# Performance work log

Hardware: AMD Instinct MI355X
Metric: run time of the kernel (lower is better)

The kernel has to match this reference:

```python
import jax, jax.numpy as jnp
import numpy as np

VOXEL = 0.1  # voxel size used in NSLoss.voxelize


def _chamfer(x, y):
    """Squared-distance chamfer terms. x: [B,N,3], y: [B,M,3].
    Returns (dist1 [B,N]: min over y for each x point, dist2 [B,M])."""
    xx = jnp.sum(x * x, axis=-1)              # [B,N]
    yy = jnp.sum(y * y, axis=-1)              # [B,M]
    zz = jnp.einsum('bnd,bmd->bnm', x, y)     # [B,N,M]
    P = xx[:, :, None] + yy[None if False else slice(None), None, :][0] if False else xx[:, :, None] + yy[:, None, :] - 2.0 * zz
    return P.min(axis=2), P.min(axis=1)


def _voxelize(coord):
    # masked_fill(nan -> inf), per-batch min over points, quantize, truncate to int
    c = jnp.where(jnp.isnan(coord), jnp.inf, coord)
    gmin = c.min(axis=1, keepdims=True)       # [B,1,3]
    grid = ((coord - gmin) / VOXEL).astype(jnp.int32)  # trunc like torch .int()
    return jax.lax.stop_gradient(grid)        # torch .int() detaches grad


def setup_inputs() -> dict:
    key = jax.random.key(0)
    k1, k2 = jax.random.split(key)
    preds = jax.random.normal(k1, (2, 8192, 3), dtype=jnp.float32)
    gts = jax.random.normal(k2, (2, 8192, 3), dtype=jnp.float32)
    return {"preds": preds, "gts": gts}


def reference(preds, gts):
    # chamfer on raw coordinates
    d1, d2 = _chamfer(preds, gts)
    loss2 = d1.mean() + d2.mean()
    # chamfer on voxelized coordinates
    pv = _voxelize(preds).astype(jnp.float32)
    gv = _voxelize(gts).astype(jnp.float32)
    d1v, d2v = _chamfer(pv, gv)
    loss1 = d1v.mean() + d2v.mean()
    return loss1 + loss2
```

## Files before the change

kernel.cpp:

```cpp
#include <hip/hip_runtime.h>
#include <math.h>

#define B 2
#define N 8192
#define PTS_STRIDE (N*3)
#define VOXEL 0.1f

#define BLK  512
#define PBLK 1024
#define XPB 64
#define XTILES (N/XPB)
#define NBLOCKS (XTILES*4)

#define WS_GMIN 0
#define WS_ACC 16
#define WS_TICKET 17
#define OFF_PACK 32
#define PERG 147456
#define OFF_AFLO(g) (OFF_PACK + (g)*PERG)
#define OFF_AFHI(g) (OFF_AFLO(g) + 32768)
#define OFF_BR(g)   (OFF_AFLO(g) + 65536)
#define OFF_BV(g)   (OFF_AFLO(g) + 98304)
#define OFF_XXR(g)  (OFF_AFLO(g) + 131072)
#define OFF_XXV(g)  (OFF_AFLO(g) + 139264)

typedef __attribute__((ext_vector_type(8))) short short8;
typedef __attribute__((ext_vector_type(16))) float f16v;

union S8 { short8 v; unsigned short u[8]; };

__device__ __forceinline__ unsigned short f2bf(float f) {
    unsigned u = __float_as_uint(f);
    return (unsigned short)((u + 0x7FFFu + ((u >> 16) & 1u)) >> 16);
}
__device__ __forceinline__ float bf2f(unsigned short h) {
    return __uint_as_float(((unsigned)h) << 16);
}
__device__ __forceinline__ float voxq(float v, float g) {
    return (float)(int)((v - g) / VOXEL);
}

__global__ void __launch_bounds__(PBLK)
gmin_kernel(const float* __restrict__ preds,
            const float* __restrict__ gts,
            float* __restrict__ ws) {
    const int g   = blockIdx.x;
    const int arr = g >> 1;
    const int b   = g & 1;
    const float* base = (arr ? gts : preds) + b * PTS_STRIDE;

    float m0 = INFINITY, m1 = INFINITY, m2 = INFINITY;
    for (int i = threadIdx.x; i < N; i += PBLK) {
        float v0 = base[i*3+0], v1 = base[i*3+1], v2 = base[i*3+2];
        v0 = (v0 != v0) ? INFINITY : v0;
        v1 = (v1 != v1) ? INFINITY : v1;
        v2 = (v2 != v2) ? INFINITY : v2;
        m0 = fminf(m0, v0); m1 = fminf(m1, v1); m2 = fminf(m2, v2);
    }
    for (int off = 32; off; off >>= 1) {
        m0 = fminf(m0, __shfl_down(m0, off));
        m1 = fminf(m1, __shfl_down(m1, off));
        m2 = fminf(m2, __shfl_down(m2, off));
    }
    __shared__ float sm[16][3];
    const int wave = threadIdx.x >> 6, lane = threadIdx.x & 63;
    if (lane == 0) { sm[wave][0] = m0; sm[wave][1] = m1; sm[wave][2] = m2; }
    __syncthreads();
    if (threadIdx.x == 0) {
        float a0 = sm[0][0], a1 = sm[0][1], a2 = sm[0][2];
        for (int w = 1; w < 16; ++w) {
            a0 = fminf(a0, sm[w][0]);
            a1 = fminf(a1, sm[w][1]);
            a2 = fminf(a2, sm[w][2]);
        }
        ws[WS_GMIN + g*3+0] = a0; ws[WS_GMIN + g*3+1] = a1; ws[WS_GMIN + g*3+2] = a2;
        if (g == 0) { ws[WS_ACC] = 0.0f; ((unsigned*)ws)[WS_TICKET] = 0u; }
    }
}

__global__ void __launch_bounds__(256)
pack_kernel(const float* __restrict__ preds,
            const float* __restrict__ gts,
            float* __restrict__ ws) {
    const int i   = blockIdx.x * 256 + threadIdx.x;
    const int g   = i >> 13;
    const int idx = i & (N-1);
    const int arr = g >> 1;
    const int b   = g & 1;
    const float* base = (arr ? gts : preds) + b * PTS_STRIDE;

    const float g0 = ws[WS_GMIN + g*3+0];
    const float g1 = ws[WS_GMIN + g*3+1];
    const float g2 = ws[WS_GMIN + g*3+2];

    const float p0 = base[idx*3+0], p1 = base[idx*3+1], p2 = base[idx*3+2];
    const float w0 = voxq(p0, g0), w1 = voxq(p1, g1), w2 = voxq(p2, g2);
    const float rr = fmaf(p0,p0, fmaf(p1,p1, p2*p2));
    const float vv = fmaf(w0,w0, fmaf(w1,w1, w2*w2));

    const unsigned short yyh = f2bf(rr);
    const unsigned short yyl = f2bf(rr - bf2f(yyh));
    const unsigned short vvh = f2bf(vv);
    const unsigned short vvl = f2bf(vv - bf2f(vvh));
    const unsigned short ONE = 0x3F80;

    short8* AFLO = (short8*)(ws + OFF_AFLO(g));
    short8* AFHI = (short8*)(ws + OFF_AFHI(g));
    short8* BR   = (short8*)(ws + OFF_BR(g));
    short8* BV   = (short8*)(ws + OFF_BV(g));

    S8 f;
    f.u[0]=f2bf(p0); f.u[1]=f2bf(p1); f.u[2]=f2bf(p2);
    f.u[3]=yyh; f.u[4]=yyl; f.u[5]=f2bf(w0); f.u[6]=f2bf(w1); f.u[7]=f2bf(w2);
    AFLO[idx] = f.v;
    f.u[0]=vvh; f.u[1]=vvl; f.u[2]=0; f.u[3]=0; f.u[4]=0; f.u[5]=0; f.u[6]=0; f.u[7]=0;
    AFHI[idx] = f.v;
    f.u[0]=f2bf(-2.0f*p0); f.u[1]=f2bf(-2.0f*p1); f.u[2]=f2bf(-2.0f*p2);
    f.u[3]=ONE; f.u[4]=ONE; f.u[5]=0; f.u[6]=0; f.u[7]=0;
    BR[idx] = f.v;
    f.u[0]=0; f.u[1]=0; f.u[2]=0; f.u[3]=0; f.u[4]=0;
    f.u[5]=f2bf(-2.0f*w0); f.u[6]=f2bf(-2.0f*w1); f.u[7]=f2bf(-2.0f*w2);
    BV[idx] = f.v;
    ws[OFF_XXR(g) + idx] = rr;
    ws[OFF_XXV(g) + idx] = vv;
}

__global__ void __launch_bounds__(BLK, 4)
chamfer_kernel(float* __restrict__ ws, float* __restrict__ out) {
    const int tid  = threadIdx.x;
    const int wave = tid >> 6, lane = tid & 63;
    const int half = lane >> 5, c32 = lane & 31;
    const int slot = blockIdx.y;
    const int dir  = slot & 1;
    const int b    = slot >> 1;
    const int gX = dir*2 + b;
    const int gY = (1-dir)*2 + b;

    const short8* ALO = (const short8*)(ws + OFF_AFLO(gY));
    const short8* AHI = (const short8*)(ws + OFF_AFHI(gY));
    const short8* Abase = half ? AHI : ALO;
    const short8* BR = (const short8*)(ws + OFF_BR(gX));
    const short8* BV = (const short8*)(ws + OFF_BV(gX));

    __shared__ float smin[8][4][32];
    __shared__ float ssum[2];

    const int xbase = blockIdx.x * XPB;
    short8 bf[4];
    S8 hc;
    hc.u[0] = (c32 < 16) ? (unsigned short)0 : (unsigned short)0x3F80;
    hc.u[1] = hc.u[0];
    hc.u[2]=0; hc.u[3]=0; hc.u[4]=0; hc.u[5]=0; hc.u[6]=0; hc.u[7]=0;
#pragma unroll
    for (int f = 0; f < 4; ++f) {
        const int xi = xbase + f*16 + (c32 & 15);
        bf[f] = (half == 0) ? ((c32 < 16) ? BR[xi] : BV[xi]) : hc.v;
    }

    float mn0 = INFINITY, mn1 = INFINITY, mn2 = INFINITY, mn3 = INFINITY;
    const f16v Z = (f16v)(0.0f);
    const int abase0 = wave * 1024 + c32;

#pragma unroll 2
    for (int t = 0; t < 32; ++t) {
        const short8 a = Abase[abase0 + t*32];
        const f16v d0 = __builtin_amdgcn_mfma_f32_32x32x16_bf16(a, bf[0], Z, 0, 0, 0);
        const f16v d1 = __builtin_amdgcn_mfma_f32_32x32x16_bf16(a, bf[1], Z, 0, 0, 0);
        const f16v d2 = __builtin_amdgcn_mfma_f32_32x32x16_bf16(a, bf[2], Z, 0, 0, 0);
        const f16v d3 = __builtin_amdgcn_mfma_f32_32x32x16_bf16(a, bf[3], Z, 0, 0, 0);
#pragma unroll
        for (int r = 0; r < 16; r += 4) {
            mn0 = fminf(mn0, fminf(fminf(d0[r], d0[r+1]), fminf(d0[r+2], d0[r+3])));
            mn1 = fminf(mn1, fminf(fminf(d1[r], d1[r+1]), fminf(d1[r+2], d1[r+3])));
            mn2 = fminf(mn2, fminf(fminf(d2[r], d2[r+1]), fminf(d2[r+2], d2[r+3])));
            mn3 = fminf(mn3, fminf(fminf(d3[r], d3[r+1]), fminf(d3[r+2], d3[r+3])));
        }
    }

    mn0 = fminf(mn0, __shfl_xor(mn0, 32));
    mn1 = fminf(mn1, __shfl_xor(mn1, 32));
    mn2 = fminf(mn2, __shfl_xor(mn2, 32));
    mn3 = fminf(mn3, __shfl_xor(mn3, 32));
    if (half == 0) {
        smin[wave][0][c32] = mn0;
        smin[wave][1][c32] = mn1;
        smin[wave][2][c32] = mn2;
        smin[wave][3][c32] = mn3;
    }
    __syncthreads();

    if (tid < 128) {
        const int f   = tid >> 5;
        const int col = tid & 31;
        float v = smin[0][f][col];
#pragma unroll
        for (int w = 1; w < 8; ++w) v = fminf(v, smin[w][f][col]);
        const int xi = xbase + f*16 + (col & 15);
        v += (col < 16) ? ws[OFF_XXR(gX) + xi] : ws[OFF_XXV(gX) + xi];
        for (int off = 32; off; off >>= 1)
            v += __shfl_down(v, off);
        if ((tid & 63) == 0) ssum[tid >> 6] = v;
    }
    __syncthreads();
    if (tid == 0) {
        const float bs = ssum[0] + ssum[1];
        atomicAdd(ws + WS_ACC, bs);
        __threadfence();
        const unsigned t = atomicAdd(&((unsigned*)ws)[WS_TICKET], 1u);
        if (t == NBLOCKS - 1) {
            __threadfence();
            const float total = atomicAdd(ws + WS_ACC, 0.0f);
            out[0] = total * (1.0f / 16384.0f);
        }
    }
}

extern "C" void kernel_launch(void* const* d_in, const int* in_sizes, int n_in,
                              void* d_out, int out_size, void* d_ws, size_t ws_size,
                              hipStream_t stream) {
    const float* preds = (const float*)d_in[0];
    const float* gts   = (const float*)d_in[1];
    float* ws  = (float*)d_ws;
    float* out = (float*)d_out;

    gmin_kernel<<<dim3(4), dim3(PBLK), 0, stream>>>(preds, gts, ws);
    pack_kernel<<<dim3(128), dim3(256), 0, stream>>>(preds, gts, ws);
    chamfer_kernel<<<dim3(XTILES, 4), dim3(BLK), 0, stream>>>(ws, out);
}
```

Before: 96.04 us.

## Split chamfer Y-range across blocks with atomicMin merge and separate finalize kernel

The chamfer kernel now uses 128-thread blocks, 32 X columns per block, and a grid split across four Y chunks. Per-column minima are merged across blocks through global atomicMin on order-preserving unsigned encodings. A new finalize kernel decodes the minima, adds the norms and reduces to the scalar loss. gmin also switches to float4 loads. The goal is more blocks and better occupancy, at the cost of global atomics, an extra launch and a larger workspace.

```diff
diff --git a/kernel.cpp b/kernel.cpp
--- a/kernel.cpp
+++ b/kernel.cpp
@@ -6,16 +6,15 @@
 #define PTS_STRIDE (N*3)
 #define VOXEL 0.1f
 
-#define BLK  512
+#define CBLK 128
 #define PBLK 1024
-#define XPB 64
-#define XTILES (N/XPB)
-#define NBLOCKS (XTILES*4)
-
-#define WS_GMIN 0
+
 #define WS_ACC 16
 #define WS_TICKET 17
-#define OFF_PACK 32
+#define WS_GMIN 20
+#define WS_MINS 32
+#define MINS_TOTAL 65536
+#define OFF_PACK (WS_MINS + MINS_TOTAL)
 #define PERG 147456
 #define OFF_AFLO(g) (OFF_PACK + (g)*PERG)
 #define OFF_AFHI(g) (OFF_AFLO(g) + 32768)
@@ -39,6 +38,14 @@
 __device__ __forceinline__ float voxq(float v, float g) {
     return (float)(int)((v - g) / VOXEL);
 }
+__device__ __forceinline__ unsigned fenc(float f) {
+    const unsigned u = __float_as_uint(f);
+    return (u & 0x80000000u) ? ~u : (u | 0x80000000u);
+}
+__device__ __forceinline__ float fdec(unsigned k) {
+    const unsigned u = (k & 0x80000000u) ? (k & 0x7FFFFFFFu) : ~k;
+    return __uint_as_float(u);
+}
 
 __global__ void __launch_bounds__(PBLK)
 gmin_kernel(const float* __restrict__ preds,
@@ -47,15 +54,28 @@
     const int g   = blockIdx.x;
     const int arr = g >> 1;
     const int b   = g & 1;
-    const float* base = (arr ? gts : preds) + b * PTS_STRIDE;
+    const float4* base4 = (const float4*)((arr ? gts : preds) + b * PTS_STRIDE);
 
     float m0 = INFINITY, m1 = INFINITY, m2 = INFINITY;
-    for (int i = threadIdx.x; i < N; i += PBLK) {
-        float v0 = base[i*3+0], v1 = base[i*3+1], v2 = base[i*3+2];
-        v0 = (v0 != v0) ? INFINITY : v0;
-        v1 = (v1 != v1) ? INFINITY : v1;
-        v2 = (v2 != v2) ? INFINITY : v2;
-        m0 = fminf(m0, v0); m1 = fminf(m1, v1); m2 = fminf(m2, v2);
+#pragma unroll
+    for (int j = 0; j < 2; ++j) {
+        const int i = j * PBLK + threadIdx.x;
+        const float4 q0 = base4[i*3+0];
+        const float4 q1 = base4[i*3+1];
+        const float4 q2 = base4[i*3+2];
+        float v;
+        v = q0.x; m0 = fminf(m0, (v!=v)?INFINITY:v);
+        v = q0.w; m0 = fminf(m0, (v!=v)?INFINITY:v);
+        v = q1.z; m0 = fminf(m0, (v!=v)?INFINITY:v);
+        v = q2.y; m0 = fminf(m0, (v!=v)?INFINITY:v);
+        v = q0.y; m1 = fminf(m1, (v!=v)?INFINITY:v);
+        v = q1.x; m1 = fminf(m1, (v!=v)?INFINITY:v);
+        v = q1.w; m1 = fminf(m1, (v!=v)?INFINITY:v);
+        v = q2.z; m1 = fminf(m1, (v!=v)?INFINITY:v);
+        v = q0.z; m2 = fminf(m2, (v!=v)?INFINITY:v);
+        v = q1.y; m2 = fminf(m2, (v!=v)?INFINITY:v);
+        v = q2.x; m2 = fminf(m2, (v!=v)?INFINITY:v);
+        v = q2.w; m2 = fminf(m2, (v!=v)?INFINITY:v);
     }
     for (int off = 32; off; off >>= 1) {
         m0 = fminf(m0, __shfl_down(m0, off));
@@ -88,6 +108,10 @@
     const int arr = g >> 1;
     const int b   = g & 1;
     const float* base = (arr ? gts : preds) + b * PTS_STRIDE;
+
+    unsigned* mins = (unsigned*)ws + WS_MINS;
+    mins[i] = 0xFF800000u;
+    mins[i + 32768] = 0xFF800000u;
 
     const float g0 = ws[WS_GMIN + g*3+0];
     const float g1 = ws[WS_GMIN + g*3+1];
@@ -125,89 +149,90 @@
     ws[OFF_XXV(g) + idx] = vv;
 }
 
-__global__ void __launch_bounds__(BLK, 4)
-chamfer_kernel(float* __restrict__ ws, float* __restrict__ out) {
+__global__ void __launch_bounds__(CBLK, 6)
+chamfer_kernel(float* __restrict__ ws) {
     const int tid  = threadIdx.x;
     const int wave = tid >> 6, lane = tid & 63;
     const int half = lane >> 5, c32 = lane & 31;
-    const int slot = blockIdx.y;
+    const int slot = blockIdx.z;
     const int dir  = slot & 1;
     const int b    = slot >> 1;
     const int gX = dir*2 + b;
     const int gY = (1-dir)*2 + b;
 
-    const short8* ALO = (const short8*)(ws + OFF_AFLO(gY));
-    const short8* AHI = (const short8*)(ws + OFF_AFHI(gY));
-    const short8* Abase = half ? AHI : ALO;
+    const short8* Abase = (const short8*)(ws + (half ? OFF_AFHI(gY) : OFF_AFLO(gY)));
     const short8* BR = (const short8*)(ws + OFF_BR(gX));
     const short8* BV = (const short8*)(ws + OFF_BV(gX));
 
-    __shared__ float smin[8][4][32];
-    __shared__ float ssum[2];
-
-    const int xbase = blockIdx.x * XPB;
-    short8 bf[4];
+    const int xbase = blockIdx.x * 32;
     S8 hc;
     hc.u[0] = (c32 < 16) ? (unsigned short)0 : (unsigned short)0x3F80;
     hc.u[1] = hc.u[0];
     hc.u[2]=0; hc.u[3]=0; hc.u[4]=0; hc.u[5]=0; hc.u[6]=0; hc.u[7]=0;
-#pragma unroll
-    for (int f = 0; f < 4; ++f) {
-        const int xi = xbase + f*16 + (c32 & 15);
-        bf[f] = (half == 0) ? ((c32 < 16) ? BR[xi] : BV[xi]) : hc.v;
-    }
-
-    float mn0 = INFINITY, mn1 = INFINITY, mn2 = INFINITY, mn3 = INFINITY;
+    const int xcol0 = xbase + (c32 & 15);
+    const short8 bf0 = (half == 0) ? ((c32 < 16) ? BR[xcol0] : BV[xcol0]) : hc.v;
+    const short8 bf1 = (half == 0) ? ((c32 < 16) ? BR[xcol0+16] : BV[xcol0+16]) : hc.v;
+
+    float mn0 = INFINITY, mn1 = INFINITY;
     const f16v Z = (f16v)(0.0f);
-    const int abase0 = wave * 1024 + c32;
+    const int abase0 = (blockIdx.y * 2 + wave) * 1024 + c32;
 
 #pragma unroll 2
     for (int t = 0; t < 32; ++t) {
         const short8 a = Abase[abase0 + t*32];
-        const f16v d0 = __builtin_amdgcn_mfma_f32_32x32x16_bf16(a, bf[0], Z, 0, 0, 0);
-        const f16v d1 = __builtin_amdgcn_mfma_f32_32x32x16_bf16(a, bf[1], Z, 0, 0, 0);
-        const f16v d2 = __builtin_amdgcn_mfma_f32_32x32x16_bf16(a, bf[2], Z, 0, 0, 0);
-        const f16v d3 = __builtin_amdgcn_mfma_f32_32x32x16_bf16(a, bf[3], Z, 0, 0, 0);
-#pragma unroll
-        for (int r = 0; r < 16; r += 4) {
-            mn0 = fminf(mn0, fminf(fminf(d0[r], d0[r+1]), fminf(d0[r+2], d0[r+3])));
-            mn1 = fminf(mn1, fminf(fminf(d1[r], d1[r+1]), fminf(d1[r+2], d1[r+3])));
-            mn2 = fminf(mn2, fminf(fminf(d2[r], d2[r+1]), fminf(d2[r+2], d2[r+3])));
-            mn3 = fminf(mn3, fminf(fminf(d3[r], d3[r+1]), fminf(d3[r+2], d3[r+3])));
+        const f16v d0 = __builtin_amdgcn_mfma_f32_32x32x16_bf16(a, bf0, Z, 0, 0, 0);
+        {
+            float t0 = fminf(fminf(d0[0], d0[1]),  fminf(d0[2], d0[3]));
+            float t1 = fminf(fminf(d0[4], d0[5]),  fminf(d0[6], d0[7]));
+            float t2 = fminf(fminf(d0[8], d0[9]),  fminf(d0[10], d0[11]));
+            float t3 = fminf(fminf(d0[12], d0[13]), fminf(d0[14], d0[15]));
+            mn0 = fminf(mn0, fminf(fminf(t0, t1), fminf(t2, t3)));
+        }
+        const f16v d1 = __builtin_amdgcn_mfma_f32_32x32x16_bf16(a, bf1, Z, 0, 0, 0);
+        {
+            float t0 = fminf(fminf(d1[0], d1[1]),  fminf(d1[2], d1[3]));
+            float t1 = fminf(fminf(d1[4], d1[5]),  fminf(d1[6], d1[7]));
+            float t2 = fminf(fminf(d1[8], d1[9]),  fminf(d1[10], d1[11]));
+            float t3 = fminf(fminf(d1[12], d1[13]), fminf(d1[14], d1[15]));
+            mn1 = fminf(mn1, fminf(fminf(t0, t1), fminf(t2, t3)));
         }
     }
 
     mn0 = fminf(mn0, __shfl_xor(mn0, 32));
     mn1 = fminf(mn1, __shfl_xor(mn1, 32));
-    mn2 = fminf(mn2, __shfl_xor(mn2, 32));
-    mn3 = fminf(mn3, __shfl_xor(mn3, 32));
+
     if (half == 0) {
-        smin[wave][0][c32] = mn0;
-        smin[wave][1][c32] = mn1;
-        smin[wave][2][c32] = mn2;
-        smin[wave][3][c32] = mn3;
-    }
+        unsigned* mins = (unsigned*)ws + WS_MINS;
+        const int var = (c32 < 16) ? 0 : 1;
+        const int e0 = ((slot*2 + var) << 13) + xcol0;
+        atomicMin(&mins[e0],      fenc(mn0));
+        atomicMin(&mins[e0 + 16], fenc(mn1));
+    }
+}
+
+__global__ void __launch_bounds__(256)
+finalize_kernel(float* __restrict__ ws, float* __restrict__ out) {
+    const int g = blockIdx.x * 256 + threadIdx.x;
+    const int slot = g >> 13;
+    const int x    = g & (N-1);
+    const int dir  = slot & 1;
+    const int b    = slot >> 1;
+    const int gX   = dir*2 + b;
+    const unsigned* mins = (const unsigned*)ws + WS_MINS;
+    float s = fdec(mins[((slot*2 + 0) << 13) + x]) + ws[OFF_XXR(gX) + x]
+            + fdec(mins[((slot*2 + 1) << 13) + x]) + ws[OFF_XXV(gX) + x];
+    for (int off = 32; off; off >>= 1)
+        s += __shfl_down(s, off);
+    __shared__ float sm[4];
+    const int wave = threadIdx.x >> 6, lane = threadIdx.x & 63;
+    if (lane == 0) sm[wave] = s;
     __syncthreads();
-
-    if (tid < 128) {
-        const int f   = tid >> 5;
-        const int col = tid & 31;
-        float v = smin[0][f][col];
-#pragma unroll
-        for (int w = 1; w < 8; ++w) v = fminf(v, smin[w][f][col]);
-        const int xi = xbase + f*16 + (col & 15);
-        v += (col < 16) ? ws[OFF_XXR(gX) + xi] : ws[OFF_XXV(gX) + xi];
-        for (int off = 32; off; off >>= 1)
-            v += __shfl_down(v, off);
-        if ((tid & 63) == 0) ssum[tid >> 6] = v;
-    }
-    __syncthreads();
-    if (tid == 0) {
-        const float bs = ssum[0] + ssum[1];
+    if (threadIdx.x == 0) {
+        const float bs = sm[0] + sm[1] + sm[2] + sm[3];
         atomicAdd(ws + WS_ACC, bs);
         __threadfence();
         const unsigned t = atomicAdd(&((unsigned*)ws)[WS_TICKET], 1u);
-        if (t == NBLOCKS - 1) {
+        if (t == gridDim.x - 1) {
             __threadfence();
             const float total = atomicAdd(ws + WS_ACC, 0.0f);
             out[0] = total * (1.0f / 16384.0f);
@@ -225,5 +250,6 @@
 
     gmin_kernel<<<dim3(4), dim3(PBLK), 0, stream>>>(preds, gts, ws);
     pack_kernel<<<dim3(128), dim3(256), 0, stream>>>(preds, gts, ws);
-    chamfer_kernel<<<dim3(XTILES, 4), dim3(BLK), 0, stream>>>(ws, out);
-}
+    chamfer_kernel<<<dim3(N/32, 4, 4), dim3(CBLK), 0, stream>>>(ws);
+    finalize_kernel<<<dim3(128), dim3(256), 0, stream>>>(ws, out);
+}
```

Result: faster. 91.01 us (-5.2%).
